# Optimization experiments

Measured on AMD Instinct MI355X. Metric: run time of the kernel, lower is better.

The kernel has to match this reference:

```python
import jax, jax.numpy as jnp
import numpy as np

K = 96  # num_scales (conv kernel width)
PAD = K // 2


def setup_inputs() -> dict:
    key = jax.random.key(0)
    kx, kh, kl = jax.random.split(key, 3)
    x = jax.random.normal(kx, (64, 128, 4096), dtype=jnp.float32)
    h_w = jax.random.normal(kh, (1, 1, K), dtype=jnp.float32) * 0.1
    l_w = jax.random.normal(kl, (1, 1, K), dtype=jnp.float32) * 0.1
    return {"x": x, "h_w": h_w, "l_w": l_w}


def reference(x, h_w, l_w):
    # Original loops over channels applying the SAME Conv1d(1,1,K) to each
    # channel slice; this is exactly a depthwise conv with a shared filter.
    # Fold channels into the batch dim and run one conv per filter.
    B, C, T = x.shape
    xr = x.reshape(B * C, 1, T)  # [B*C, 1, T]

    def conv(w):
        # torch Conv1d is cross-correlation; lax conv matches (no kernel flip)
        y = jax.lax.conv_general_dilated(
            xr, w, window_strides=(1,), padding=[(PAD, PAD)],
            dimension_numbers=("NCH", "OIH", "NCH"))
        return y.reshape(B, C, -1)  # [B, C, T+1] for even K

    l_outs = conv(l_w)
    h_outs = conv(h_w)
    return (l_outs, h_outs)
```

## Files before the change

kernel.cpp:

```cpp
#include <hip/hip_runtime.h>


#define KW    96
#define PADW  48
#define T_IN  4096
#define T_OUT 4097
#define ROWS  8192
#define TILE  2048
#define RPT   8
#define BLOCK 256
#define SPAN  (TILE + 96)
#define SPAN4 (SPAN / 4)

__global__ __launch_bounds__(BLOCK) void lwt_kernel(
    const float* __restrict__ x,
    const float* __restrict__ hw,
    const float* __restrict__ lw,
    float* __restrict__ out_l,
    float* __restrict__ out_h)
{
    __shared__ alignas(16) float lds[SPAN];
    const int bid = blockIdx.x;
    const int tid = threadIdx.x;

    if (bid < ROWS * 2) {
        const int row = bid >> 1;
        const int t0  = (bid & 1) * TILE;
        const float* xrow = x + (size_t)row * T_IN;
        const int g0 = t0 - PADW;

        float4* L4 = (float4*)lds;
        for (int i = tid; i < SPAN4; i += BLOCK) {
            const int g = g0 + 4 * i;
            float4 v = make_float4(0.f, 0.f, 0.f, 0.f);
            if (g >= 0 && g < T_IN) v = *(const float4*)(xrow + g);
            L4[i] = v;
        }
        __syncthreads();

        float accl[RPT], acch[RPT];
        #pragma unroll
        for (int i = 0; i < RPT; ++i) { accl[i] = 0.f; acch[i] = 0.f; }

        const int base4 = tid * 2;
        float4 A  = L4[base4];
        float4 Bv = L4[base4 + 1];
        #pragma unroll
        for (int s = 0; s < KW / 4; ++s) {
            const float4 Cv = L4[base4 + 2 + s];
            const float win[12] = {A.x, A.y, A.z, A.w,
                                   Bv.x, Bv.y, Bv.z, Bv.w,
                                   Cv.x, Cv.y, Cv.z, Cv.w};
            #pragma unroll
            for (int q = 0; q < 4; ++q) {
                const int k = 4 * s + q;
                const float wl = lw[k];
                const float wh = hw[k];
                #pragma unroll
                for (int i = 0; i < RPT; ++i) {
                    accl[i] = fmaf(win[q + i], wl, accl[i]);
                    acch[i] = fmaf(win[q + i], wh, acch[i]);
                }
            }
            A = Bv; Bv = Cv;
        }
        __syncthreads();

        const size_t obase = (size_t)row * T_OUT + t0;
        #pragma unroll
        for (int i = 0; i < RPT; ++i) lds[tid * RPT + i] = accl[i];
        __syncthreads();
        for (int j = tid; j < TILE; j += BLOCK) out_l[obase + j] = lds[j];
        __syncthreads();
        #pragma unroll
        for (int i = 0; i < RPT; ++i) lds[tid * RPT + i] = acch[i];
        __syncthreads();
        for (int j = tid; j < TILE; j += BLOCK) out_h[obase + j] = lds[j];
    } else {
        const int r = (bid - ROWS * 2) * BLOCK + tid;
        if (r < ROWS) {
            const float* xp = x + (size_t)r * T_IN + (T_OUT - 1 - PADW);
            float al = 0.f, ah = 0.f;
            #pragma unroll
            for (int k = 0; k < PADW; ++k) {
                const float xv = xp[k];
                al = fmaf(xv, lw[k], al);
                ah = fmaf(xv, hw[k], ah);
            }
            const size_t o = (size_t)r * T_OUT + (T_OUT - 1);
            out_l[o] = al;
            out_h[o] = ah;
        }
    }
}

extern "C" void kernel_launch(void* const* d_in, const int* in_sizes, int n_in,
                              void* d_out, int out_size, void* d_ws, size_t ws_size,
                              hipStream_t stream) {
    const float* x  = (const float*)d_in[0];
    const float* hw = (const float*)d_in[1];
    const float* lw = (const float*)d_in[2];
    float* out_l = (float*)d_out;
    float* out_h = out_l + (size_t)ROWS * T_OUT;

    const int grid = ROWS * 2 + (ROWS + BLOCK - 1) / BLOCK;
    lwt_kernel<<<grid, BLOCK, 0, stream>>>(x, hw, lw, out_l, out_h);
}
```

Before: 455.6 us.

## Recast shared-filter conv as bf16 MFMA Toeplitz matmul

Replaces the scalar FMA sliding-window convolution with bf16 MFMA 16x16x32 instructions. A small init kernel packs both filters into a shifted Toeplitz-style B operand in workspace, and the input tile is converted to bf16 in LDS. Results pass through a padded LDS bounce buffer for coalesced stores. This moves the compute onto matrix cores but lowers input and weight precision to bf16, which may exceed the accuracy tolerance.

Measured after the change: 367.5 us. 1.24x faster.

```diff
diff --git a/kernel.cpp b/kernel.cpp
--- a/kernel.cpp
+++ b/kernel.cpp
@@ -6,76 +6,117 @@
 #define T_IN  4096
 #define T_OUT 4097
 #define ROWS  8192
-#define TILE  2048
-#define RPT   8
+#define TT    2048
+#define NTILE 16
 #define BLOCK 256
-#define SPAN  (TILE + 96)
-#define SPAN4 (SPAN / 4)
+#define NF4   544
+#define XSH   (NF4 * 4)
+#define BREG  2320
 
-__global__ __launch_bounds__(BLOCK) void lwt_kernel(
+typedef __attribute__((ext_vector_type(8))) short short8;
+typedef __attribute__((ext_vector_type(4))) float f32x4;
+
+__device__ __forceinline__ unsigned short f2bf(float v) {
+    unsigned u = __builtin_bit_cast(unsigned, v);
+    u += 0x7FFFu + ((u >> 16) & 1u);
+    return (unsigned short)(u >> 16);
+}
+
+__global__ __launch_bounds__(BLOCK) void lwt_init(
+    const float* __restrict__ hw, const float* __restrict__ lw,
+    unsigned short* __restrict__ ws)
+{
+    const int t = threadIdx.x;
+    const int L = t >> 2, c = t & 3;
+    const int n = L & 15, q = L >> 4;
+    const int s = n & 7, f = n >> 3;
+    const float* w = f ? hw : lw;
+    unsigned short b[8];
+    #pragma unroll
+    for (int j = 0; j < 8; ++j) {
+        const int k = 32 * c + 8 * q + j;
+        const int kk = k - s;
+        b[j] = (kk >= 0 && kk < KW) ? f2bf(w[kk]) : (unsigned short)0;
+    }
+    uint4 pk;
+    pk.x = (unsigned)b[0] | ((unsigned)b[1] << 16);
+    pk.y = (unsigned)b[2] | ((unsigned)b[3] << 16);
+    pk.z = (unsigned)b[4] | ((unsigned)b[5] << 16);
+    pk.w = (unsigned)b[6] | ((unsigned)b[7] << 16);
+    ((uint4*)ws)[t] = pk;
+}
+
+__global__ __launch_bounds__(BLOCK) void lwt_main(
     const float* __restrict__ x,
     const float* __restrict__ hw,
     const float* __restrict__ lw,
+    const unsigned short* __restrict__ ws,
     float* __restrict__ out_l,
     float* __restrict__ out_h)
 {
-    __shared__ alignas(16) float lds[SPAN];
+    __shared__ alignas(16) unsigned short xs[XSH];
+    __shared__ float bounce[2 * BREG];
     const int bid = blockIdx.x;
     const int tid = threadIdx.x;
 
     if (bid < ROWS * 2) {
         const int row = bid >> 1;
-        const int t0  = (bid & 1) * TILE;
+        const int T0  = (bid & 1) * TT;
         const float* xrow = x + (size_t)row * T_IN;
-        const int g0 = t0 - PADW;
 
-        float4* L4 = (float4*)lds;
-        for (int i = tid; i < SPAN4; i += BLOCK) {
-            const int g = g0 + 4 * i;
+        for (int i = tid; i < NF4; i += BLOCK) {
+            const int g = T0 - PADW + 4 * i;
             float4 v = make_float4(0.f, 0.f, 0.f, 0.f);
             if (g >= 0 && g < T_IN) v = *(const float4*)(xrow + g);
-            L4[i] = v;
+            ushort4 u;
+            u.x = f2bf(v.x); u.y = f2bf(v.y); u.z = f2bf(v.z); u.w = f2bf(v.w);
+            *(ushort4*)(xs + 4 * i) = u;
+        }
+
+        const int lane = tid & 63;
+        const short8* wsB = (const short8*)ws;
+        short8 bf0 = wsB[lane * 4 + 0];
+        short8 bf1 = wsB[lane * 4 + 1];
+        short8 bf2 = wsB[lane * 4 + 2];
+        short8 bf3 = wsB[lane * 4 + 3];
+        __syncthreads();
+
+        const int wv = tid >> 6;
+        const int m  = lane & 15;
+        const int q  = lane >> 4;
+        const int nD = lane & 15;
+        const int sD = nD & 7;
+        const int fD = nD >> 3;
+        const short8* ap = (const short8*)xs;
+
+        #pragma unroll
+        for (int it = 0; it < 4; ++it) {
+            const int tile = wv * 4 + it;
+            const int ga0 = tile * 16 + m + q;
+            f32x4 acc = {0.f, 0.f, 0.f, 0.f};
+            acc = __builtin_amdgcn_mfma_f32_16x16x32_bf16(ap[ga0     ], bf0, acc, 0, 0, 0);
+            acc = __builtin_amdgcn_mfma_f32_16x16x32_bf16(ap[ga0 +  4], bf1, acc, 0, 0, 0);
+            acc = __builtin_amdgcn_mfma_f32_16x16x32_bf16(ap[ga0 +  8], bf2, acc, 0, 0, 0);
+            acc = __builtin_amdgcn_mfma_f32_16x16x32_bf16(ap[ga0 + 12], bf3, acc, 0, 0, 0);
+            #pragma unroll
+            for (int r = 0; r < 4; ++r) {
+                const int i0 = tile * 128 + 32 * q + 8 * r + sD;
+                bounce[fD * BREG + i0 + (i0 >> 3)] = acc[r];
+            }
         }
         __syncthreads();
 
-        float accl[RPT], acch[RPT];
+        const size_t ob = (size_t)row * T_OUT + T0;
         #pragma unroll
-        for (int i = 0; i < RPT; ++i) { accl[i] = 0.f; acch[i] = 0.f; }
-
-        const int base4 = tid * 2;
-        float4 A  = L4[base4];
-        float4 Bv = L4[base4 + 1];
+        for (int rep = 0; rep < TT / BLOCK; ++rep) {
+            const int i = tid + rep * BLOCK;
+            out_l[ob + i] = bounce[i + (i >> 3)];
+        }
         #pragma unroll
-        for (int s = 0; s < KW / 4; ++s) {
-            const float4 Cv = L4[base4 + 2 + s];
-            const float win[12] = {A.x, A.y, A.z, A.w,
-                                   Bv.x, Bv.y, Bv.z, Bv.w,
-                                   Cv.x, Cv.y, Cv.z, Cv.w};
-            #pragma unroll
-            for (int q = 0; q < 4; ++q) {
-                const int k = 4 * s + q;
-                const float wl = lw[k];
-                const float wh = hw[k];
-                #pragma unroll
-                for (int i = 0; i < RPT; ++i) {
-                    accl[i] = fmaf(win[q + i], wl, accl[i]);
-                    acch[i] = fmaf(win[q + i], wh, acch[i]);
-                }
-            }
-            A = Bv; Bv = Cv;
+        for (int rep = 0; rep < TT / BLOCK; ++rep) {
+            const int i = tid + rep * BLOCK;
+            out_h[ob + i] = bounce[BREG + i + (i >> 3)];
         }
-        __syncthreads();
-
-        const size_t obase = (size_t)row * T_OUT + t0;
-        #pragma unroll
-        for (int i = 0; i < RPT; ++i) lds[tid * RPT + i] = accl[i];
-        __syncthreads();
-        for (int j = tid; j < TILE; j += BLOCK) out_l[obase + j] = lds[j];
-        __syncthreads();
-        #pragma unroll
-        for (int i = 0; i < RPT; ++i) lds[tid * RPT + i] = acch[i];
-        __syncthreads();
-        for (int j = tid; j < TILE; j += BLOCK) out_h[obase + j] = lds[j];
     } else {
         const int r = (bid - ROWS * 2) * BLOCK + tid;
         if (r < ROWS) {
@@ -102,7 +143,9 @@
     const float* lw = (const float*)d_in[2];
     float* out_l = (float*)d_out;
     float* out_h = out_l + (size_t)ROWS * T_OUT;
+    unsigned short* wsB = (unsigned short*)d_ws;
 
-    const int grid = ROWS * 2 + (ROWS + BLOCK - 1) / BLOCK;
-    lwt_kernel<<<grid, BLOCK, 0, stream>>>(x, hw, lw, out_l, out_h);
+    lwt_init<<<1, BLOCK, 0, stream>>>(hw, lw, wsB);
+    const int grid = ROWS * 2 + ROWS / BLOCK;
+    lwt_main<<<grid, BLOCK, 0, stream>>>(x, hw, lw, wsB, out_l, out_h);
 }
```
